# Kernel optimization log

Hardware: AMD Instinct MI355X
Metric: run time of the kernel (lower is better)

## Reference

```python
import jax, jax.numpy as jnp
import numpy as np

N_ITER = 50  # default n_iter of entmax.entmax_bisect


def entmax_bisect(X, alpha, n_iter=N_ITER):
    """alpha-entmax over the last axis via bisection (entmax package algorithm)."""
    d = X.shape[-1]
    am1 = alpha - 1.0
    inv = 1.0 / am1
    Xa = X * am1

    def p(z):  # clamp(z,0)**(1/(alpha-1)), grad-safe at 0
        return jnp.where(z > 0, jnp.maximum(z, 1e-30) ** inv, 0.0)

    max_val = jnp.max(Xa, axis=-1, keepdims=True)
    tau_lo = max_val - 1.0                       # _gp(1, alpha) = 1
    tau_hi = max_val - (1.0 / d) ** am1          # _gp(1/d, alpha)
    f_lo = jnp.sum(p(Xa - tau_lo), axis=-1, keepdims=True) - 1.0
    dm0 = tau_hi - tau_lo

    def body(carry, _):
        tau_lo, dm, _ = carry
        dm = dm * 0.5
        tau_m = tau_lo + dm
        f_m = jnp.sum(p(Xa - tau_m), axis=-1, keepdims=True) - 1.0
        tau_lo = jnp.where(f_m * f_lo >= 0, tau_m, tau_lo)
        return (tau_lo, dm, tau_m), None

    (_, _, tau_m), _ = jax.lax.scan(body, (tau_lo, dm0, tau_lo), None, length=n_iter)
    pm = p(Xa - tau_m)
    return pm / jnp.sum(pm, axis=-1, keepdims=True)  # ensure_sum_one=True


def setup_inputs() -> dict:
    key = jax.random.key(0)
    ks = jax.random.split(key, 10)
    b, c, e, h = 8, 2048, 64, 8
    s_in = 1.0 / np.sqrt(e)
    s_u = 1.0 / np.sqrt(h * e)
    x = jax.random.normal(ks[0], (b, c, e), jnp.float32)
    Wk = jax.random.normal(ks[1], (h * e, e), jnp.float32) * s_in
    bk = jax.random.normal(ks[2], (h * e,), jnp.float32) * 0.01
    Wq = jax.random.normal(ks[3], (h * e, e), jnp.float32) * s_in
    bq = jax.random.normal(ks[4], (h * e,), jnp.float32) * 0.01
    Wv = jax.random.normal(ks[5], (h * e, e), jnp.float32) * s_in
    bv = jax.random.normal(ks[6], (h * e,), jnp.float32) * 0.01
    Wu = jax.random.normal(ks[7], (e, h * e), jnp.float32) * s_u
    bu = jax.random.normal(ks[8], (e,), jnp.float32) * 0.01
    alpha = jnp.asarray(1.5, jnp.float32)  # learned scalar
    return dict(x=x, alpha=alpha, Wk=Wk, bk=bk, Wq=Wq, bq=bq,
                Wv=Wv, bv=bv, Wu=Wu, bu=bu)


def reference(x, alpha, Wk, bk, Wq, bq, Wv, bv, Wu, bu):
    b, c, e = x.shape
    h = Wk.shape[0] // e
    k = (x @ Wk.T + bk).reshape(b, c, h, e)
    q = (x @ Wq.T + bq).reshape(b, c, h, e)
    v = (x @ Wv.T + bv).reshape(b, c, h, e)
    # dot[b,c,i,j] = sum_h q[b,c,h,i] * k[b,c,h,j] / sqrt(e)   (per-token e x e scores)
    dot = jnp.einsum('bchi,bchj->bcij', q, k) / np.sqrt(e).astype(np.float32)
    att = entmax_bisect(dot, alpha)
    # res[b,c,h,i] = sum_j att[b,c,i,j] * v[b,c,h,j]
    res = jnp.einsum('bcij,bchj->bchi', att, v).reshape(b, c, h * e)
    return res @ Wu.T + bu
```

## Files before the change

kernel.cpp:

```cpp
#include <hip/hip_runtime.h>
#include <math.h>

#define NTOK 16384
#define EDIM 64
#define HHE  512
#define TOKPAD 260

typedef _Float16 half8 __attribute__((ext_vector_type(8)));
typedef __fp16   half2v __attribute__((ext_vector_type(2)));
typedef float    floatx4 __attribute__((ext_vector_type(4)));

__device__ __forceinline__ half8 cvt8(const float4 a, const float4 b) {
    half8 h;
    h[0] = (_Float16)a.x; h[1] = (_Float16)a.y;
    h[2] = (_Float16)a.z; h[3] = (_Float16)a.w;
    h[4] = (_Float16)b.x; h[5] = (_Float16)b.y;
    h[6] = (_Float16)b.z; h[7] = (_Float16)b.w;
    return h;
}

__device__ __forceinline__ float dot2(half2v a, half2v b, float c) {
#if __has_builtin(__builtin_amdgcn_fdot2)
    return __builtin_amdgcn_fdot2(a, b, c, false);
#else
    return fmaf((float)a[0], (float)b[0], fmaf((float)a[1], (float)b[1], c));
#endif
}
__device__ __forceinline__ half2v pk(float x, float y) {
    return __builtin_amdgcn_cvt_pkrtz(x, y);
}
union h2u { half2v h; unsigned int u; };

__device__ __forceinline__ float clamp01(float z) {
    return __builtin_amdgcn_fmed3f(z, 0.0f, 1.0f);
}
__device__ __forceinline__ float pgen(float z, float inv) {
    return z > 0.0f ? exp2f(inv * log2f(fmaxf(z, 1e-30f))) : 0.0f;
}

__global__ __launch_bounds__(256) void cvt_fp16_kernel(
    const float* __restrict__ x,
    const float* __restrict__ Wk, const float* __restrict__ Wq,
    const float* __restrict__ Wv, const float* __restrict__ Wu,
    __fp16* __restrict__ xh, __fp16* __restrict__ wkh,
    __fp16* __restrict__ wqh, __fp16* __restrict__ wvh,
    __fp16* __restrict__ wuh)
{
    const int z = blockIdx.y;
    const float* src; __fp16* dst; int n;
    if      (z == 0) { src = x;  dst = xh;  n = NTOK * EDIM; }
    else if (z == 1) { src = Wk; dst = wkh; n = HHE * EDIM; }
    else if (z == 2) { src = Wq; dst = wqh; n = HHE * EDIM; }
    else if (z == 3) { src = Wv; dst = wvh; n = HHE * EDIM; }
    else             { src = Wu; dst = wuh; n = EDIM * HHE; }
    const int idx = (blockIdx.x * 256 + threadIdx.x) * 8;
    if (idx < n) {
        const float4 a = *(const float4*)(src + idx);
        const float4 b = *(const float4*)(src + idx + 4);
        *(half8*)(dst + idx) = cvt8(a, b);
    }
}

__global__ __launch_bounds__(256) void qkv_attn_kernel(
    const __fp16* __restrict__ xh,
    const __fp16* __restrict__ wkh, const float* __restrict__ bk,
    const __fp16* __restrict__ wqh, const float* __restrict__ bq,
    const __fp16* __restrict__ wvh, const float* __restrict__ bv,
    __fp16* __restrict__ resb, const float* alpha_p)
{
    __shared__ __align__(16) half2v qT[16 * TOKPAD];
    __shared__ __align__(16) half2v kT[16 * TOKPAD];
    __shared__ __align__(16) half2v vT[16 * TOKPAD];

    const int tid  = threadIdx.x;
    const int lane = tid & 63;
    const int w    = tid >> 6;
    const int tok0 = blockIdx.x * 16;

    const int m    = lane & 15;
    const int quad = lane >> 4;

    const __fp16* xrow = xh + (size_t)(tok0 + m) * EDIM + quad * 8;
    half8 bfr[2];
    bfr[0] = *(const half8*)(xrow);
    bfr[1] = *(const half8*)(xrow + 32);

    #pragma unroll
    for (int uu = 0; uu < 3; ++uu) {
        const int unit = w * 3 + uu;
        const int z    = unit >> 2;
        const int col0 = (unit & 3) * 128;
        const __fp16* W   = (z == 0) ? wkh : (z == 1) ? wqh : wvh;
        const float* bias = (z == 0) ? bk : (z == 1) ? bq : bv;
        half2v* dstT      = (z == 0) ? kT : (z == 1) ? qT : vT;

        #pragma unroll
        for (int ct = 0; ct < 8; ++ct) {
            const int n = col0 + ct * 16 + m;
            const int grow = (z < 2) ? ((n & 7) * 64 + (n >> 3)) : n;
            const __fp16* wrow = W + (size_t)grow * EDIM + quad * 8;
            floatx4 acc = (floatx4){0.f, 0.f, 0.f, 0.f};
            #pragma unroll
            for (int kc = 0; kc < 2; ++kc) {
                const half8 af = *(const half8*)(wrow + kc * 32);
                acc = __builtin_amdgcn_mfma_f32_16x16x32_f16(af, bfr[kc], acc, 0, 0, 0);
            }
            h2u p0, p1;
            if (z < 2) {
                const int hbase = 4 * (quad & 1);
                const int j     = (col0 >> 3) + ct * 2 + (quad >> 1);
                float o0 = acc[0] + bias[(hbase + 0) * 64 + j];
                float o1 = acc[1] + bias[(hbase + 1) * 64 + j];
                float o2 = acc[2] + bias[(hbase + 2) * 64 + j];
                float o3 = acc[3] + bias[(hbase + 3) * 64 + j];
                p0.h = pk(o0, o1);
                p1.h = pk(o2, o3);
                uint2 st; st.x = p0.u; st.y = p1.u;
                *(uint2*)&dstT[m * TOKPAD + j * 4 + 2 * (quad & 1)] = st;
            } else {
                const int nn = col0 + ct * 16 + quad * 4;
                const int h  = nn >> 6;
                const int jj = nn & 63;
                const float4 b4 = *(const float4*)&bias[nn];
                p0.h = pk(acc[0] + b4.x, acc[1] + b4.y);
                p1.h = pk(acc[2] + b4.z, acc[3] + b4.w);
                uint2 st; st.x = p0.u; st.y = p1.u;
                *(uint2*)&dstT[m * TOKPAD + h * 32 + (jj >> 1)] = st;
            }
        }
    }
    __syncthreads();

    const float alpha = alpha_p[0];
    const float am1   = alpha - 1.0f;

    for (int i = 0; i < 4; ++i) {
        const int t   = w * 4 + i;
        const int tok = tok0 + t;

        union { half8 h8; half2v h2[4]; } uq;
        uq.h8 = *(const half8*)&qT[t * TOKPAD + lane * 4];

        float row[64];
        #pragma unroll
        for (int j = 0; j < 64; ++j) {
            union { half8 h8; half2v h2[4]; } u;
            u.h8 = *(const half8*)&kT[t * TOKPAD + j * 4];
            float d = dot2(uq.h2[0], u.h2[0], 0.0f);
            d = dot2(uq.h2[1], u.h2[1], d);
            d = dot2(uq.h2[2], u.h2[2], d);
            d = dot2(uq.h2[3], u.h2[3], d);
            row[j] = d;
        }

        const float scale = am1 * 0.125f;
        #pragma unroll
        for (int j = 0; j < 64; ++j) row[j] *= scale;

        float mx = row[0];
        #pragma unroll
        for (int j = 1; j < 64; ++j) mx = fmaxf(mx, row[j]);

        float tau_lo = mx - 1.0f;
        const float tau_hi = mx - exp2f(-6.0f * am1);
        float dm = tau_hi - tau_lo;
        float inv_sum;

        if (am1 == 0.5f) {
            #pragma unroll
            for (int it = 0; it < 6; ++it) {
                dm *= 0.5f;
                const float tau_m = tau_lo + dm;
                float f0 = -1.0f, f1 = 0.0f, f2 = 0.0f, f3 = 0.0f;
                #pragma unroll
                for (int j = 0; j < 64; j += 4) {
                    const float a0 = clamp01(row[j+0] - tau_m);
                    const float a1 = clamp01(row[j+1] - tau_m);
                    const float a2 = clamp01(row[j+2] - tau_m);
                    const float a3 = clamp01(row[j+3] - tau_m);
                    f0 = fmaf(a0, a0, f0); f1 = fmaf(a1, a1, f1);
                    f2 = fmaf(a2, a2, f2); f3 = fmaf(a3, a3, f3);
                }
                const float f = (f0 + f1) + (f2 + f3);
                tau_lo = (f >= 0.0f) ? tau_m : tau_lo;
            }
            float tau = tau_lo;
            #pragma unroll
            for (int it = 0; it < 2; ++it) {
                float f0 = -1.0f, f1 = 0.0f, f2 = 0.0f, f3 = 0.0f;
                float s0 = 0.0f, s1 = 0.0f, s2 = 0.0f, s3 = 0.0f;
                #pragma unroll
                for (int j = 0; j < 64; j += 4) {
                    const float a0 = clamp01(row[j+0] - tau);
                    const float a1 = clamp01(row[j+1] - tau);
                    const float a2 = clamp01(row[j+2] - tau);
                    const float a3 = clamp01(row[j+3] - tau);
                    f0 = fmaf(a0, a0, f0); f1 = fmaf(a1, a1, f1);
                    f2 = fmaf(a2, a2, f2); f3 = fmaf(a3, a3, f3);
                    s0 += a0; s1 += a1; s2 += a2; s3 += a3;
                }
                const float f = (f0 + f1) + (f2 + f3);
                const float s = ((s0 + s1) + (s2 + s3)) + 1e-20f;
                tau = tau + fmaxf(f, 0.0f) / (s + s);
            }
            float s0 = 0.0f, s1 = 0.0f;
            #pragma unroll
            for (int j = 0; j < 64; j += 2) {
                float a0 = clamp01(row[j+0] - tau);
                float a1 = clamp01(row[j+1] - tau);
                a0 *= a0; a1 *= a1;
                row[j+0] = a0; row[j+1] = a1;
                s0 += a0; s1 += a1;
            }
            inv_sum = 1.0f / (s0 + s1);
        } else {
            const float inv = 1.0f / am1;
            float tau_m = tau_lo;
            float f_lo = -1.0f;
            #pragma unroll
            for (int j = 0; j < 64; ++j) f_lo += pgen(row[j] - tau_lo, inv);
            for (int it = 0; it < 30; ++it) {
                dm *= 0.5f;
                tau_m = tau_lo + dm;
                float f = -1.0f;
                #pragma unroll
                for (int j = 0; j < 64; ++j) f += pgen(row[j] - tau_m, inv);
                tau_lo = (f * f_lo >= 0.0f) ? tau_m : tau_lo;
            }
            float s = 0.0f;
            #pragma unroll
            for (int j = 0; j < 64; ++j) {
                const float pm = pgen(row[j] - tau_m, inv);
                row[j] = pm;
                s += pm;
            }
            inv_sum = 1.0f / s;
        }

        half2v p2[32];
        #pragma unroll
        for (int ii = 0; ii < 32; ++ii) p2[ii] = pk(row[2 * ii], row[2 * ii + 1]);

        float acc[8];
        #pragma unroll
        for (int h = 0; h < 8; ++h) {
            float a0 = 0.0f, a1 = 0.0f;
            #pragma unroll
            for (int jc = 0; jc < 8; ++jc) {
                union { half8 h8; half2v h2[4]; } u;
                u.h8 = *(const half8*)&vT[t * TOKPAD + h * 32 + jc * 4];
                a0 = dot2(p2[jc * 4 + 0], u.h2[0], a0);
                a1 = dot2(p2[jc * 4 + 1], u.h2[1], a1);
                a0 = dot2(p2[jc * 4 + 2], u.h2[2], a0);
                a1 = dot2(p2[jc * 4 + 3], u.h2[3], a1);
            }
            acc[h] = a0 + a1;
        }
        __fp16* rp = resb + (size_t)tok * HHE;
        #pragma unroll
        for (int h = 0; h < 8; ++h) rp[h * 64 + lane] = (__fp16)(acc[h] * inv_sum);
    }
}

__global__ __launch_bounds__(256) void out_kernel(
    const __fp16* __restrict__ resh, const __fp16* __restrict__ wuh,
    const float* __restrict__ bu, float* __restrict__ out)
{
    const int tid  = threadIdx.x;
    const int lane = tid & 63;
    const int w    = tid >> 6;
    const int m    = lane & 15;
    const int quad = lane >> 4;

    const int tok0 = blockIdx.x * 32 + (w >> 1) * 16;
    const int ctb  = (w & 1) * 2;

    floatx4 acc[2];
    acc[0] = (floatx4){0.f, 0.f, 0.f, 0.f};
    acc[1] = (floatx4){0.f, 0.f, 0.f, 0.f};

    const __fp16* rrow = resh + (size_t)(tok0 + m) * HHE + quad * 8;

    #pragma unroll
    for (int kc = 0; kc < 16; ++kc) {
        const half8 bf = *(const half8*)(rrow + kc * 32);
        #pragma unroll
        for (int c = 0; c < 2; ++c) {
            const int n = (ctb + c) * 16 + m;
            const half8 af =
                *(const half8*)(wuh + (size_t)n * HHE + kc * 32 + quad * 8);
            acc[c] = __builtin_amdgcn_mfma_f32_16x16x32_f16(af, bf, acc[c], 0, 0, 0);
        }
    }

    const int tok = tok0 + m;
    #pragma unroll
    for (int c = 0; c < 2; ++c) {
        const int col = (ctb + c) * 16 + quad * 4;
        const float4 b4 = *(const float4*)&bu[col];
        float4 o;
        o.x = acc[c][0] + b4.x;
        o.y = acc[c][1] + b4.y;
        o.z = acc[c][2] + b4.z;
        o.w = acc[c][3] + b4.w;
        *(float4*)&out[(size_t)tok * 64 + col] = o;
    }
}

extern "C" void kernel_launch(void* const* d_in, const int* in_sizes, int n_in,
                              void* d_out, int out_size, void* d_ws, size_t ws_size,
                              hipStream_t stream)
{
    const float* x     = (const float*)d_in[0];
    const float* alpha = (const float*)d_in[1];
    const float* Wk    = (const float*)d_in[2];
    const float* bk    = (const float*)d_in[3];
    const float* Wq    = (const float*)d_in[4];
    const float* bq    = (const float*)d_in[5];
    const float* Wv    = (const float*)d_in[6];
    const float* bv    = (const float*)d_in[7];
    const float* Wu    = (const float*)d_in[8];
    const float* bu    = (const float*)d_in[9];
    float* out = (float*)d_out;

    __fp16* xh   = (__fp16*)d_ws;
    __fp16* wkh  = xh  + (size_t)NTOK * EDIM;
    __fp16* wqh  = wkh + (size_t)HHE * EDIM;
    __fp16* wvh  = wqh + (size_t)HHE * EDIM;
    __fp16* wuh  = wvh + (size_t)HHE * EDIM;
    __fp16* resb = wuh + (size_t)EDIM * HHE;

    cvt_fp16_kernel<<<dim3(512, 5), 256, 0, stream>>>(
        x, Wk, Wq, Wv, Wu, xh, wkh, wqh, wvh, wuh);
    qkv_attn_kernel<<<NTOK / 16, 256, 0, stream>>>(
        xh, wkh, bk, wqh, bq, wvh, bv, resb, alpha);
    out_kernel<<<NTOK / 32, 256, 0, stream>>>(resb, wuh, bu, out);
}
```

Baseline: 168.2 us.

## Fuse output projection into attention kernel via LDS-resident result tile

```diff
diff --git a/kernel.cpp b/kernel.cpp
--- a/kernel.cpp
+++ b/kernel.cpp
@@ -61,12 +61,13 @@
     }
 }
 
-__global__ __launch_bounds__(256) void qkv_attn_kernel(
+__global__ __launch_bounds__(256) void qkv_attn_out_kernel(
     const __fp16* __restrict__ xh,
     const __fp16* __restrict__ wkh, const float* __restrict__ bk,
     const __fp16* __restrict__ wqh, const float* __restrict__ bq,
     const __fp16* __restrict__ wvh, const float* __restrict__ bv,
-    __fp16* __restrict__ resb, const float* alpha_p)
+    const __fp16* __restrict__ wuh, const float* __restrict__ bu,
+    float* __restrict__ out, const float* alpha_p)
 {
     __shared__ __align__(16) half2v qT[16 * TOKPAD];
     __shared__ __align__(16) half2v kT[16 * TOKPAD];
@@ -133,10 +134,10 @@
 
     const float alpha = alpha_p[0];
     const float am1   = alpha - 1.0f;
+    __fp16* resL = (__fp16*)qT;
 
     for (int i = 0; i < 4; ++i) {
-        const int t   = w * 4 + i;
-        const int tok = tok0 + t;
+        const int t = w * 4 + i;
 
         union { half8 h8; half2v h2[4]; } uq;
         uq.h8 = *(const half8*)&qT[t * TOKPAD + lane * 4];
@@ -256,53 +257,30 @@
             }
             acc[h] = a0 + a1;
         }
-        __fp16* rp = resb + (size_t)tok * HHE;
-        #pragma unroll
-        for (int h = 0; h < 8; ++h) rp[h * 64 + lane] = (__fp16)(acc[h] * inv_sum);
+        #pragma unroll
+        for (int h = 0; h < 8; ++h)
+            resL[t * 520 + h * 64 + lane] = (__fp16)(acc[h] * inv_sum);
     }
-}
-
-__global__ __launch_bounds__(256) void out_kernel(
-    const __fp16* __restrict__ resh, const __fp16* __restrict__ wuh,
-    const float* __restrict__ bu, float* __restrict__ out)
-{
-    const int tid  = threadIdx.x;
-    const int lane = tid & 63;
-    const int w    = tid >> 6;
-    const int m    = lane & 15;
-    const int quad = lane >> 4;
-
-    const int tok0 = blockIdx.x * 32 + (w >> 1) * 16;
-    const int ctb  = (w & 1) * 2;
-
-    floatx4 acc[2];
-    acc[0] = (floatx4){0.f, 0.f, 0.f, 0.f};
-    acc[1] = (floatx4){0.f, 0.f, 0.f, 0.f};
-
-    const __fp16* rrow = resh + (size_t)(tok0 + m) * HHE + quad * 8;
-
-    #pragma unroll
-    for (int kc = 0; kc < 16; ++kc) {
-        const half8 bf = *(const half8*)(rrow + kc * 32);
-        #pragma unroll
-        for (int c = 0; c < 2; ++c) {
-            const int n = (ctb + c) * 16 + m;
-            const half8 af =
-                *(const half8*)(wuh + (size_t)n * HHE + kc * 32 + quad * 8);
-            acc[c] = __builtin_amdgcn_mfma_f32_16x16x32_f16(af, bf, acc[c], 0, 0, 0);
-        }
-    }
-
-    const int tok = tok0 + m;
-    #pragma unroll
-    for (int c = 0; c < 2; ++c) {
-        const int col = (ctb + c) * 16 + quad * 4;
+    __syncthreads();
+
+    {
+        floatx4 oacc = (floatx4){0.f, 0.f, 0.f, 0.f};
+        const __fp16* rrow = resL + (size_t)m * 520 + quad * 8;
+        const __fp16* wrow = wuh + (size_t)(w * 16 + m) * HHE + quad * 8;
+        #pragma unroll
+        for (int kc = 0; kc < 16; ++kc) {
+            const half8 bf = *(const half8*)(rrow + kc * 32);
+            const half8 af = *(const half8*)(wrow + kc * 32);
+            oacc = __builtin_amdgcn_mfma_f32_16x16x32_f16(af, bf, oacc, 0, 0, 0);
+        }
+        const int tok = tok0 + m;
+        const int col = w * 16 + quad * 4;
         const float4 b4 = *(const float4*)&bu[col];
         float4 o;
-        o.x = acc[c][0] + b4.x;
-        o.y = acc[c][1] + b4.y;
-        o.z = acc[c][2] + b4.z;
-        o.w = acc[c][3] + b4.w;
+        o.x = oacc[0] + b4.x;
+        o.y = oacc[1] + b4.y;
+        o.z = oacc[2] + b4.z;
+        o.w = oacc[3] + b4.w;
         *(float4*)&out[(size_t)tok * 64 + col] = o;
     }
 }
@@ -328,11 +306,9 @@
     __fp16* wqh  = wkh + (size_t)HHE * EDIM;
     __fp16* wvh  = wqh + (size_t)HHE * EDIM;
     __fp16* wuh  = wvh + (size_t)HHE * EDIM;
-    __fp16* resb = wuh + (size_t)EDIM * HHE;
 
     cvt_fp16_kernel<<<dim3(512, 5), 256, 0, stream>>>(
         x, Wk, Wq, Wv, Wu, xh, wkh, wqh, wvh, wuh);
-    qkv_attn_kernel<<<NTOK / 16, 256, 0, stream>>>(
-        xh, wkh, bk, wqh, bq, wvh, bv, resb, alpha);
-    out_kernel<<<NTOK / 32, 256, 0, stream>>>(resb, wuh, bu, out);
-}
+    qkv_attn_out_kernel<<<NTOK / 16, 256, 0, stream>>>(
+        xh, wkh, bk, wqh, bq, wvh, bv, wuh, bu, out, alpha);
+}
```

New measurement: 156.3 us (median of 2 runs). 7.1% less time.
